# Performance work log

Hardware: AMD Instinct MI355X
Metric: run time of the kernel (lower is better)

Reference implementation:

```python
import jax, jax.numpy as jnp
import numpy as np

EPS = jnp.float16(1e-8)

def setup_inputs() -> dict:
    key = jax.random.key(0)
    k1, k2, k3, k4 = jax.random.split(key, 4)
    B, S, D_IN, D_OUT = 4, 2048, 4096, 4096
    x = jax.random.normal(k1, (B, S, D_IN), dtype=jnp.float16)
    weight = jax.random.randint(k2, (D_OUT, D_IN), -127, 127, dtype=jnp.int32).astype(jnp.int8)
    weight_scales = (jax.random.uniform(k3, (D_OUT,), dtype=jnp.float32) * 0.02 + 0.001).astype(jnp.float16)
    bias = (jax.random.normal(k4, (1, D_OUT), dtype=jnp.float32) * 0.01).astype(jnp.float16)
    return {"x": x, "weight": weight, "weight_scales": weight_scales, "bias": bias}

def fake_quant_per_token(x):
    # per-token absmax fake quant to int8 range, stays fp16
    scales = jnp.max(jnp.abs(x), axis=-1, keepdims=True) / jnp.float16(127.0)
    scales = jnp.maximum(scales, EPS)
    return jnp.round(x / scales) * scales

def reference(x, weight, weight_scales, bias):
    # dequantize int8 weight with per-output-channel scales -> fp16 [out, in]
    w_fp16 = weight.astype(jnp.float16) * weight_scales[:, None]
    xq = fake_quant_per_token(x)
    # y = xq @ w^T + bias  : [B, S, out]
    y = jnp.einsum('bsi,oi->bso', xq, w_fp16) + bias
    return y
```

## Files before the change

### kernel.cpp

```cpp
#include <hip/hip_runtime.h>
#include <hip/hip_fp16.h>
#include <stdint.h>

#define M_TOK 8192
#define KD 4096
#define ND 4096

using i32x4 = __attribute__((ext_vector_type(4))) int;
using f32x4 = __attribute__((ext_vector_type(4))) float;

typedef const __attribute__((address_space(1))) void* gp_t;
typedef __attribute__((address_space(3))) void* lp_t;

__global__ __launch_bounds__(256) void prep_kernel(
    const float* __restrict__ x,
    int8_t* __restrict__ q,
    float* __restrict__ scales,
    const int* __restrict__ w32,
    int8_t* __restrict__ w8)
{
    const int t = threadIdx.x;
    if (blockIdx.x >= 8192) {
        const int b = blockIdx.x - 8192;
        const int4* w4 = (const int4*)w32;
        int* q32 = (int*)w8;
        #pragma unroll
        for (int u = 0; u < 4; ++u) {
            int g = b * 1024 + u * 256 + t;
            int4 a = w4[g];
            q32[g] = (a.x & 255) | ((a.y & 255) << 8) | ((a.z & 255) << 16) | (a.w << 24);
        }
        return;
    }

    const int row  = blockIdx.x;
    const int lane = t & 63;
    const int wave = t >> 6;

    const float4* xr = (const float4*)(x + (size_t)row * KD);
    float4 p[4];
    #pragma unroll
    for (int i = 0; i < 4; ++i) p[i] = xr[i * 256 + t];

    float am = 0.0f;
    #pragma unroll
    for (int i = 0; i < 4; ++i) {
        am = fmaxf(am, fmaxf(fmaxf(fabsf(p[i].x), fabsf(p[i].y)),
                             fmaxf(fabsf(p[i].z), fabsf(p[i].w))));
    }
    #pragma unroll
    for (int off = 32; off >= 1; off >>= 1)
        am = fmaxf(am, __shfl_xor(am, off));

    __shared__ float smax[4];
    if (lane == 0) smax[wave] = am;
    __syncthreads();
    am = fmaxf(fmaxf(smax[0], smax[1]), fmaxf(smax[2], smax[3]));

    float s = __half2float(__float2half(am * (1.0f / 127.0f)));
    s = fmaxf(s, 1e-30f);
    const float inv = 1.0f / s;

    int* qr = (int*)(q + (size_t)row * KD);
    #pragma unroll
    for (int i = 0; i < 4; ++i) {
        float vv[4] = {p[i].x, p[i].y, p[i].z, p[i].w};
        int w32v = 0;
        #pragma unroll
        for (int e = 0; e < 4; ++e) {
            float tq = __half2float(__float2half(vv[e] * inv));
            int qi = (int)rintf(tq);
            qi = max(-127, min(127, qi));
            w32v |= (qi & 255) << (8 * e);
        }
        qr[i * 256 + t] = w32v;
    }
    if (t == 0) scales[row] = s;
}


__device__ __forceinline__ void read_Af(const char* lA, int wr, int lane, i32x4 (&a)[4][2]) {
    const int l15 = lane & 15;
    const int cg  = (lane >> 4) << 4;
    #pragma unroll
    for (int mf = 0; mf < 4; ++mf) {
        const int row = wr * 64 + mf * 16 + l15;
        const int sw  = (row & 7) << 4;
        #pragma unroll
        for (int ks = 0; ks < 2; ++ks)
            a[mf][ks] = *(const i32x4*)(lA + row * 128 + ((ks * 64 + cg) ^ sw));
    }
}

__device__ __forceinline__ void read_Bf(const char* lB, int wc, int lane, i32x4 (&b)[4][2]) {
    const int l15 = lane & 15;
    const int cg  = (lane >> 4) << 4;
    #pragma unroll
    for (int nf = 0; nf < 4; ++nf) {
        const int row = wc * 64 + nf * 16 + l15;
        const int sw  = (row & 7) << 4;
        #pragma unroll
        for (int ks = 0; ks < 2; ++ks)
            b[nf][ks] = *(const i32x4*)(lB + row * 128 + ((ks * 64 + cg) ^ sw));
    }
}

__device__ __forceinline__ void mfma_32(i32x4 (&acc)[4][4],
                                        const i32x4 (&a)[4][2],
                                        const i32x4 (&b)[4][2]) {
    __builtin_amdgcn_s_setprio(1);
    #pragma unroll
    for (int ks = 0; ks < 2; ++ks)
        #pragma unroll
        for (int mf = 0; mf < 4; ++mf)
            #pragma unroll
            for (int nf = 0; nf < 4; ++nf)
                acc[mf][nf] = __builtin_amdgcn_mfma_i32_16x16x64_i8(a[mf][ks], b[nf][ks],
                                                                    acc[mf][nf], 0, 0, 0);
    __builtin_amdgcn_s_setprio(0);
}

#define BAR()   __builtin_amdgcn_s_barrier()
#define LGKM0() asm volatile("s_waitcnt lgkmcnt(0)" ::: "memory")
#define VM8()   asm volatile("s_waitcnt vmcnt(8)")

__global__ __launch_bounds__(256, 2) void gemm_q8_128_kernel(
    const int8_t* __restrict__ q,
    const int8_t* __restrict__ w8,
    const float* __restrict__ qs,
    const float* __restrict__ wscale,
    const float* __restrict__ bias,
    float* __restrict__ y)
{
    __shared__ char lds[2][2][16384];

    const int tid  = threadIdx.x;
    const int lane = tid & 63;
    const int wave = tid >> 6;
    const int wr   = wave >> 1;
    const int wc   = wave & 1;
    const int tn   = blockIdx.x;
    const int tm   = blockIdx.y;

    const int8_t* gA = q  + (size_t)(tm * 128) * KD;
    const int8_t* gB = w8 + (size_t)(tn * 128) * KD;

    char* lA0 = &lds[0][0][0]; char* lB0 = &lds[0][1][0];
    char* lA1 = &lds[1][0][0]; char* lB1 = &lds[1][1][0];

    int goff[4];
    #pragma unroll
    for (int ch = 0; ch < 4; ++ch) {
        const int d = ch * 4096 + tid * 16;
        const int r = d >> 7;
        const int cs = (d & 127) ^ ((r & 7) << 4);
        goff[ch] = r * KD + cs;
    }
    const int ldso = tid * 16;

    #define STAGE(gbase, kbyte, ldst)                                                    \
        do {                                                                             \
            const int8_t* _s = (gbase) + (kbyte);                                        \
            __builtin_amdgcn_global_load_lds((gp_t)(_s + goff[0]), (lp_t)((ldst) + ldso),            16, 0, 0); \
            __builtin_amdgcn_global_load_lds((gp_t)(_s + goff[1]), (lp_t)((ldst) + 4096 + ldso),     16, 0, 0); \
            __builtin_amdgcn_global_load_lds((gp_t)(_s + goff[2]), (lp_t)((ldst) + 8192 + ldso),     16, 0, 0); \
            __builtin_amdgcn_global_load_lds((gp_t)(_s + goff[3]), (lp_t)((ldst) + 12288 + ldso),    16, 0, 0); \
        } while (0)

    i32x4 acc[4][4] = {};
    i32x4 a[4][2], b[4][2];

    STAGE(gA, 0,   lA0);
    STAGE(gB, 0,   lB0);
    STAGE(gA, 128, lA1);
    STAGE(gB, 128, lB1);
    VM8();
    BAR();

    for (int it = 0; it < 16; ++it) {
        const int kt  = 2 * it;
        const int kb2 = ((kt + 2) & 31) * 128;
        const int kb3 = ((kt + 3) & 31) * 128;

        read_Af(lA0, wr, lane, a);
        read_Bf(lB0, wc, lane, b);
        LGKM0();
        BAR();
        STAGE(gA, kb2, lA0);
        STAGE(gB, kb2, lB0);
        mfma_32(acc, a, b);
        VM8();
        BAR();

        read_Af(lA1, wr, lane, a);
        read_Bf(lB1, wc, lane, b);
        LGKM0();
        BAR();
        STAGE(gA, kb3, lA1);
        STAGE(gB, kb3, lB1);
        mfma_32(acc, a, b);
        VM8();
        BAR();
    }
    asm volatile("s_waitcnt vmcnt(0)");
    BAR();

    {
        char* myl = &lds[0][0][0] + wave * 16384;
        const int g   = lane >> 4;
        const int l15 = lane & 15;
        #pragma unroll
        for (int mf = 0; mf < 4; ++mf) {
            const int rmb = tm * 128 + wr * 64 + mf * 16 + g * 4;
            float qsv[4];
            #pragma unroll
            for (int r = 0; r < 4; ++r) qsv[r] = qs[rmb + r];
            #pragma unroll
            for (int nf = 0; nf < 4; ++nf) {
                const int n  = tn * 128 + wc * 64 + nf * 16 + l15;
                const float wn = wscale[n];
                const float bn = bias[n];
                const int cl = nf * 16 + l15;
                #pragma unroll
                for (int r = 0; r < 4; ++r) {
                    const int rl = mf * 16 + g * 4 + r;
                    const float val = (float)acc[mf][nf][r] * (qsv[r] * wn) + bn;
                    *(float*)(myl + rl * 256 + ((cl * 4) ^ ((rl & 7) << 4))) = val;
                }
            }
        }
        __builtin_amdgcn_s_barrier();
        const int gcol = tn * 128 + wc * 64 + l15 * 4;
        #pragma unroll
        for (int k = 0; k < 16; ++k) {
            const int rl = g + k * 4;
            const f32x4 v = *(const f32x4*)(myl + rl * 256 + ((l15 * 16) ^ ((rl & 7) << 4)));
            const int grow = tm * 128 + wr * 64 + rl;
            __builtin_nontemporal_store(v, (f32x4*)(y + (size_t)grow * ND + gcol));
        }
    }
    #undef STAGE
}

__global__ __launch_bounds__(256, 2) void gemm_q8_fallback(
    const int8_t* __restrict__ q,
    const int* __restrict__ w32,
    const float* __restrict__ qs,
    const float* __restrict__ wscale,
    const float* __restrict__ bias,
    float* __restrict__ y)
{
    __shared__ int8_t lA[128 * 64];
    __shared__ int8_t lB[128 * 64];

    const int tid  = threadIdx.x;
    const int lane = tid & 63;
    const int wave = tid >> 6;
    const int wr   = wave >> 1;
    const int wc   = wave & 1;
    const int tn   = blockIdx.x;
    const int tm   = blockIdx.y;

    const int ci0  = wave * 2;
    const int off0 = ci0 * 1024 + lane * 16;
    const int r0   = off0 >> 6;
    const int c0   = off0 & 63;
    const int off1 = off0 + 1024;
    const int r1   = off1 >> 6;
    const int c1   = off1 & 63;

    const int8_t* gA0 = q + (size_t)(tm * 128 + r0) * KD + c0;
    const int8_t* gA1 = q + (size_t)(tm * 128 + r1) * KD + c1;

    const int brow  = tid >> 1;
    const int bhalf = tid & 1;
    const int* gW = w32 + (size_t)(tn * 128 + brow) * KD + bhalf * 32;

    i32x4 acc[4][4] = {};
    const int kc = (lane >> 4) * 16;
    const int rA = wr * 64 + (lane & 15);
    const int rB = wc * 64 + (lane & 15);

    for (int k0 = 0; k0 < KD; k0 += 64) {
        __builtin_amdgcn_global_load_lds((gp_t)(gA0 + k0), (lp_t)(lA + ci0 * 1024),        16, 0, 0);
        __builtin_amdgcn_global_load_lds((gp_t)(gA1 + k0), (lp_t)(lA + ci0 * 1024 + 1024), 16, 0, 0);
        int bw[8];
        #pragma unroll
        for (int u = 0; u < 8; ++u) {
            i32x4 a4 = *(const i32x4*)(gW + k0 + u * 4);
            bw[u] = (a4[0] & 255) | ((a4[1] & 255) << 8) | ((a4[2] & 255) << 16) | (a4[3] << 24);
        }
        *(i32x4*)(lB + brow * 64 + bhalf * 32)      = i32x4{bw[0], bw[1], bw[2], bw[3]};
        *(i32x4*)(lB + brow * 64 + bhalf * 32 + 16) = i32x4{bw[4], bw[5], bw[6], bw[7]};
        __syncthreads();

        i32x4 a[4], b[4];
        #pragma unroll
        for (int i = 0; i < 4; ++i) a[i] = *(const i32x4*)(lA + (rA + i * 16) * 64 + kc);
        #pragma unroll
        for (int j = 0; j < 4; ++j) b[j] = *(const i32x4*)(lB + (rB + j * 16) * 64 + kc);
        #pragma unroll
        for (int i = 0; i < 4; ++i)
            #pragma unroll
            for (int j = 0; j < 4; ++j)
                acc[i][j] = __builtin_amdgcn_mfma_i32_16x16x64_i8(a[i], b[j], acc[i][j], 0, 0, 0);
        __syncthreads();
    }

    const int cbase = tn * 128 + wc * 64 + (lane & 15);
    const int rbase = tm * 128 + wr * 64 + ((lane >> 4) << 2);
    #pragma unroll
    for (int j = 0; j < 4; ++j) {
        const int n  = cbase + j * 16;
        const float wn = wscale[n];
        const float bn = bias[n];
        #pragma unroll
        for (int i = 0; i < 4; ++i)
            #pragma unroll
            for (int r = 0; r < 4; ++r) {
                const int m = rbase + i * 16 + r;
                y[(size_t)m * ND + n] = (float)acc[i][j][r] * (qs[m] * wn) + bn;
            }
    }
}

extern "C" void kernel_launch(void* const* d_in, const int* in_sizes, int n_in,
                              void* d_out, int out_size, void* d_ws, size_t ws_size,
                              hipStream_t stream) {
    const float* x      = (const float*)d_in[0];
    const int*   w32    = (const int*)d_in[1];
    const float* wscale = (const float*)d_in[2];
    const float* bias   = (const float*)d_in[3];
    float*       y      = (float*)d_out;

    const size_t q_bytes  = (size_t)M_TOK * KD;
    const size_t s_bytes  = (size_t)M_TOK * sizeof(float);
    const size_t w8_bytes = (size_t)ND * KD;

    int8_t* qbuf   = (int8_t*)d_ws;
    float*  scales = (float*)((char*)d_ws + q_bytes);
    int8_t* w8     = (int8_t*)((char*)d_ws + q_bytes + s_bytes);

    if (ws_size >= q_bytes + s_bytes + w8_bytes) {
        prep_kernel<<<8192 + 4096, 256, 0, stream>>>(x, qbuf, scales, w32, w8);
        dim3 grid(ND / 128, M_TOK / 128);
        gemm_q8_128_kernel<<<grid, 256, 0, stream>>>(qbuf, w8, scales, wscale, bias, y);
    } else {
        prep_kernel<<<8192, 256, 0, stream>>>(x, qbuf, scales, w32, w8);
        dim3 grid(ND / 128, M_TOK / 128);
        gemm_q8_fallback<<<grid, 256, 0, stream>>>(qbuf, w32, scales, wscale, bias, y);
    }
}
```

Before: 174.0 us.

## Enlarge GEMM tile to 256x128 with K=64 stages and swizzled block order

```diff
diff --git a/kernel.cpp b/kernel.cpp
--- a/kernel.cpp
+++ b/kernel.cpp
@@ -79,52 +79,23 @@
 }
 
 
-__device__ __forceinline__ void read_Af(const char* lA, int wr, int lane, i32x4 (&a)[4][2]) {
-    const int l15 = lane & 15;
-    const int cg  = (lane >> 4) << 4;
-    #pragma unroll
-    for (int mf = 0; mf < 4; ++mf) {
-        const int row = wr * 64 + mf * 16 + l15;
-        const int sw  = (row & 7) << 4;
-        #pragma unroll
-        for (int ks = 0; ks < 2; ++ks)
-            a[mf][ks] = *(const i32x4*)(lA + row * 128 + ((ks * 64 + cg) ^ sw));
-    }
-}
-
-__device__ __forceinline__ void read_Bf(const char* lB, int wc, int lane, i32x4 (&b)[4][2]) {
-    const int l15 = lane & 15;
-    const int cg  = (lane >> 4) << 4;
-    #pragma unroll
-    for (int nf = 0; nf < 4; ++nf) {
-        const int row = wc * 64 + nf * 16 + l15;
-        const int sw  = (row & 7) << 4;
-        #pragma unroll
-        for (int ks = 0; ks < 2; ++ks)
-            b[nf][ks] = *(const i32x4*)(lB + row * 128 + ((ks * 64 + cg) ^ sw));
-    }
-}
-
-__device__ __forceinline__ void mfma_32(i32x4 (&acc)[4][4],
-                                        const i32x4 (&a)[4][2],
-                                        const i32x4 (&b)[4][2]) {
+__device__ __forceinline__ void mfma_32(i32x4 (&acc)[8][4],
+                                        const i32x4 (&a)[8],
+                                        const i32x4 (&b)[4]) {
     __builtin_amdgcn_s_setprio(1);
     #pragma unroll
-    for (int ks = 0; ks < 2; ++ks)
-        #pragma unroll
-        for (int mf = 0; mf < 4; ++mf)
-            #pragma unroll
-            for (int nf = 0; nf < 4; ++nf)
-                acc[mf][nf] = __builtin_amdgcn_mfma_i32_16x16x64_i8(a[mf][ks], b[nf][ks],
-                                                                    acc[mf][nf], 0, 0, 0);
+    for (int mf = 0; mf < 8; ++mf)
+        #pragma unroll
+        for (int nf = 0; nf < 4; ++nf)
+            acc[mf][nf] = __builtin_amdgcn_mfma_i32_16x16x64_i8(a[mf], b[nf], acc[mf][nf], 0, 0, 0);
     __builtin_amdgcn_s_setprio(0);
 }
 
 #define BAR()   __builtin_amdgcn_s_barrier()
 #define LGKM0() asm volatile("s_waitcnt lgkmcnt(0)" ::: "memory")
-#define VM8()   asm volatile("s_waitcnt vmcnt(8)")
-
-__global__ __launch_bounds__(256, 2) void gemm_q8_128_kernel(
+#define VM6()   asm volatile("s_waitcnt vmcnt(6)")
+
+__global__ __launch_bounds__(256, 2) void gemm_q8_hrb_kernel(
     const int8_t* __restrict__ q,
     const int8_t* __restrict__ w8,
     const float* __restrict__ qs,
@@ -132,114 +103,155 @@
     const float* __restrict__ bias,
     float* __restrict__ y)
 {
-    __shared__ char lds[2][2][16384];
+    __shared__ char lds[2][24576];
 
     const int tid  = threadIdx.x;
     const int lane = tid & 63;
     const int wave = tid >> 6;
     const int wr   = wave >> 1;
     const int wc   = wave & 1;
-    const int tn   = blockIdx.x;
-    const int tm   = blockIdx.y;
-
-    const int8_t* gA = q  + (size_t)(tm * 128) * KD;
+
+    const int bid = blockIdx.x;
+    const int sid = (bid & 7) * 128 + (bid >> 3);
+    const int tn  = sid & 31;
+    const int tm  = sid >> 5;
+
+    const int8_t* gA = q  + (size_t)(tm * 256) * KD;
     const int8_t* gB = w8 + (size_t)(tn * 128) * KD;
 
-    char* lA0 = &lds[0][0][0]; char* lB0 = &lds[0][1][0];
-    char* lA1 = &lds[1][0][0]; char* lB1 = &lds[1][1][0];
+    const int l15 = lane & 15;
+    const int cg  = (lane >> 4) << 4;
+    const int swz = ((l15 >> 1) & 7) << 4;
+    const int c0  = (cg + 64 * (l15 & 1)) ^ swz;
+    unsigned aoff[8], boff[4];
+    #pragma unroll
+    for (int mf = 0; mf < 8; ++mf)
+        aoff[mf] = (unsigned)((wr * 64 + mf * 8 + (l15 >> 1)) * 128 + c0);
+    #pragma unroll
+    for (int nf = 0; nf < 4; ++nf)
+        boff[nf] = (unsigned)((wc * 32 + nf * 8 + (l15 >> 1)) * 128 + c0);
 
     int goff[4];
     #pragma unroll
     for (int ch = 0; ch < 4; ++ch) {
-        const int d = ch * 4096 + tid * 16;
-        const int r = d >> 7;
-        const int cs = (d & 127) ^ ((r & 7) << 4);
-        goff[ch] = r * KD + cs;
+        const int d  = ch * 4096 + tid * 16;
+        const int i  = d >> 7;
+        const int sp = (d >> 4) & 7;
+        const int s  = sp ^ (i & 7);
+        const int r  = 2 * i + (s >> 2);
+        const int k  = (s & 3) * 16;
+        goff[ch] = r * KD + k;
     }
     const int ldso = tid * 16;
 
-    #define STAGE(gbase, kbyte, ldst)                                                    \
+    #define STAGE(kbyte, buf)                                                                         \
+        do {                                                                                          \
+            char* _lA = &lds[buf][0];                                                                 \
+            char* _lB = &lds[buf][16384];                                                             \
+            __builtin_amdgcn_global_load_lds((gp_t)(gA + (kbyte) + goff[0]), (lp_t)(_lA + ldso),          16, 0, 0); \
+            __builtin_amdgcn_global_load_lds((gp_t)(gA + (kbyte) + goff[1]), (lp_t)(_lA + 4096 + ldso),   16, 0, 0); \
+            __builtin_amdgcn_global_load_lds((gp_t)(gA + (kbyte) + goff[2]), (lp_t)(_lA + 8192 + ldso),   16, 0, 0); \
+            __builtin_amdgcn_global_load_lds((gp_t)(gA + (kbyte) + goff[3]), (lp_t)(_lA + 12288 + ldso),  16, 0, 0); \
+            __builtin_amdgcn_global_load_lds((gp_t)(gB + (kbyte) + goff[0]), (lp_t)(_lB + ldso),          16, 0, 0); \
+            __builtin_amdgcn_global_load_lds((gp_t)(gB + (kbyte) + goff[1]), (lp_t)(_lB + 4096 + ldso),   16, 0, 0); \
+        } while (0)
+
+    #define READS(buf)                                                                   \
         do {                                                                             \
-            const int8_t* _s = (gbase) + (kbyte);                                        \
-            __builtin_amdgcn_global_load_lds((gp_t)(_s + goff[0]), (lp_t)((ldst) + ldso),            16, 0, 0); \
-            __builtin_amdgcn_global_load_lds((gp_t)(_s + goff[1]), (lp_t)((ldst) + 4096 + ldso),     16, 0, 0); \
-            __builtin_amdgcn_global_load_lds((gp_t)(_s + goff[2]), (lp_t)((ldst) + 8192 + ldso),     16, 0, 0); \
-            __builtin_amdgcn_global_load_lds((gp_t)(_s + goff[3]), (lp_t)((ldst) + 12288 + ldso),    16, 0, 0); \
+            const char* _lA = &lds[buf][0];                                              \
+            const char* _lB = &lds[buf][16384];                                          \
+            _Pragma("unroll")                                                            \
+            for (int mf = 0; mf < 8; ++mf) a[mf] = *(const i32x4*)(_lA + aoff[mf]);      \
+            _Pragma("unroll")                                                            \
+            for (int nf = 0; nf < 4; ++nf) b[nf] = *(const i32x4*)(_lB + boff[nf]);      \
         } while (0)
 
-    i32x4 acc[4][4] = {};
-    i32x4 a[4][2], b[4][2];
-
-    STAGE(gA, 0,   lA0);
-    STAGE(gB, 0,   lB0);
-    STAGE(gA, 128, lA1);
-    STAGE(gB, 128, lB1);
-    VM8();
-    BAR();
-
-    for (int it = 0; it < 16; ++it) {
-        const int kt  = 2 * it;
-        const int kb2 = ((kt + 2) & 31) * 128;
-        const int kb3 = ((kt + 3) & 31) * 128;
-
-        read_Af(lA0, wr, lane, a);
-        read_Bf(lB0, wc, lane, b);
+    i32x4 acc[8][4] = {};
+    i32x4 a[8], b[4];
+
+    STAGE(0,  0);
+    STAGE(64, 1);
+    VM6();
+    BAR();
+
+    for (int it = 0; it < 31; ++it) {
+        const int kb2 = (2 * it + 2) * 64;
+        const int kb3 = (2 * it + 3) * 64;
+
+        READS(0);
         LGKM0();
         BAR();
-        STAGE(gA, kb2, lA0);
-        STAGE(gB, kb2, lB0);
+        STAGE(kb2, 0);
         mfma_32(acc, a, b);
-        VM8();
+        VM6();
         BAR();
 
-        read_Af(lA1, wr, lane, a);
-        read_Bf(lB1, wc, lane, b);
+        READS(1);
         LGKM0();
         BAR();
-        STAGE(gA, kb3, lA1);
-        STAGE(gB, kb3, lB1);
+        STAGE(kb3, 1);
         mfma_32(acc, a, b);
-        VM8();
+        VM6();
         BAR();
     }
+
+    READS(0);
+    LGKM0();
+    BAR();
+    mfma_32(acc, a, b);
     asm volatile("s_waitcnt vmcnt(0)");
     BAR();
 
+    READS(1);
+    LGKM0();
+    BAR();
+    mfma_32(acc, a, b);
+    BAR();
+
     {
-        char* myl = &lds[0][0][0] + wave * 16384;
-        const int g   = lane >> 4;
-        const int l15 = lane & 15;
-        #pragma unroll
-        for (int mf = 0; mf < 4; ++mf) {
-            const int rmb = tm * 128 + wr * 64 + mf * 16 + g * 4;
-            float qsv[4];
-            #pragma unroll
-            for (int r = 0; r < 4; ++r) qsv[r] = qs[rmb + r];
-            #pragma unroll
-            for (int nf = 0; nf < 4; ++nf) {
-                const int n  = tn * 128 + wc * 64 + nf * 16 + l15;
-                const float wn = wscale[n];
-                const float bn = bias[n];
-                const int cl = nf * 16 + l15;
+        char* eld = &lds[0][0];
+        const int g = lane >> 4;
+        #pragma unroll
+        for (int p = 0; p < 4; ++p) {
+            if (wr == (p >> 1)) {
                 #pragma unroll
-                for (int r = 0; r < 4; ++r) {
-                    const int rl = mf * 16 + g * 4 + r;
-                    const float val = (float)acc[mf][nf][r] * (qsv[r] * wn) + bn;
-                    *(float*)(myl + rl * 256 + ((cl * 4) ^ ((rl & 7) << 4))) = val;
+                for (int mq = 0; mq < 4; ++mq) {
+                    const int mf  = (p & 1) * 4 + mq;
+                    const int rmb = tm * 256 + wr * 128 + mf * 16 + g * 4;
+                    float qsv[4];
+                    #pragma unroll
+                    for (int r = 0; r < 4; ++r) qsv[r] = qs[rmb + r];
+                    #pragma unroll
+                    for (int nf = 0; nf < 4; ++nf) {
+                        const int n  = tn * 128 + wc * 64 + nf * 16 + l15;
+                        const float wn = wscale[n];
+                        const float bn = bias[n];
+                        const int cl = wc * 64 + nf * 16 + l15;
+                        #pragma unroll
+                        for (int r = 0; r < 4; ++r) {
+                            const int rl = mq * 16 + g * 4 + r;
+                            const float val = (float)acc[mf][nf][r] * (qsv[r] * wn) + bn;
+                            *(float*)(eld + rl * 512 + ((cl * 4) ^ ((rl & 31) << 4))) = val;
+                        }
+                    }
                 }
             }
+            __builtin_amdgcn_s_barrier();
+            const int c32 = tid & 31;
+            const int r8  = tid >> 5;
+            const int gcol = tn * 128 + c32 * 4;
+            #pragma unroll
+            for (int k = 0; k < 8; ++k) {
+                const int rl = r8 + k * 8;
+                const f32x4 v = *(const f32x4*)(eld + rl * 512 + ((c32 * 16) ^ ((rl & 31) << 4)));
+                const int grow = tm * 256 + p * 64 + rl;
+                __builtin_nontemporal_store(v, (f32x4*)(y + (size_t)grow * ND + gcol));
+            }
+            __builtin_amdgcn_s_barrier();
         }
-        __builtin_amdgcn_s_barrier();
-        const int gcol = tn * 128 + wc * 64 + l15 * 4;
-        #pragma unroll
-        for (int k = 0; k < 16; ++k) {
-            const int rl = g + k * 4;
-            const f32x4 v = *(const f32x4*)(myl + rl * 256 + ((l15 * 16) ^ ((rl & 7) << 4)));
-            const int grow = tm * 128 + wr * 64 + rl;
-            __builtin_nontemporal_store(v, (f32x4*)(y + (size_t)grow * ND + gcol));
-        }
     }
     #undef STAGE
+    #undef READS
 }
 
 __global__ __launch_bounds__(256, 2) void gemm_q8_fallback(
@@ -343,8 +355,7 @@
 
     if (ws_size >= q_bytes + s_bytes + w8_bytes) {
         prep_kernel<<<8192 + 4096, 256, 0, stream>>>(x, qbuf, scales, w32, w8);
-        dim3 grid(ND / 128, M_TOK / 128);
-        gemm_q8_128_kernel<<<grid, 256, 0, stream>>>(qbuf, w8, scales, wscale, bias, y);
+        gemm_q8_hrb_kernel<<<1024, 256, 0, stream>>>(qbuf, w8, scales, wscale, bias, y);
     } else {
         prep_kernel<<<8192, 256, 0, stream>>>(x, qbuf, scales, w32, w8);
         dim3 grid(ND / 128, M_TOK / 128);
```

New measurement: 185.5 us. 1.07x slower.

## Restructure int8 GEMM mainloop into triple-buffered K=64 pipeline with register prefetch

Applied to the files above, without the earlier changes.

```diff
diff --git a/kernel.cpp b/kernel.cpp
--- a/kernel.cpp
+++ b/kernel.cpp
@@ -79,52 +79,9 @@
 }
 
 
-__device__ __forceinline__ void read_Af(const char* lA, int wr, int lane, i32x4 (&a)[4][2]) {
-    const int l15 = lane & 15;
-    const int cg  = (lane >> 4) << 4;
-    #pragma unroll
-    for (int mf = 0; mf < 4; ++mf) {
-        const int row = wr * 64 + mf * 16 + l15;
-        const int sw  = (row & 7) << 4;
-        #pragma unroll
-        for (int ks = 0; ks < 2; ++ks)
-            a[mf][ks] = *(const i32x4*)(lA + row * 128 + ((ks * 64 + cg) ^ sw));
-    }
-}
-
-__device__ __forceinline__ void read_Bf(const char* lB, int wc, int lane, i32x4 (&b)[4][2]) {
-    const int l15 = lane & 15;
-    const int cg  = (lane >> 4) << 4;
-    #pragma unroll
-    for (int nf = 0; nf < 4; ++nf) {
-        const int row = wc * 64 + nf * 16 + l15;
-        const int sw  = (row & 7) << 4;
-        #pragma unroll
-        for (int ks = 0; ks < 2; ++ks)
-            b[nf][ks] = *(const i32x4*)(lB + row * 128 + ((ks * 64 + cg) ^ sw));
-    }
-}
-
-__device__ __forceinline__ void mfma_32(i32x4 (&acc)[4][4],
-                                        const i32x4 (&a)[4][2],
-                                        const i32x4 (&b)[4][2]) {
-    __builtin_amdgcn_s_setprio(1);
-    #pragma unroll
-    for (int ks = 0; ks < 2; ++ks)
-        #pragma unroll
-        for (int mf = 0; mf < 4; ++mf)
-            #pragma unroll
-            for (int nf = 0; nf < 4; ++nf)
-                acc[mf][nf] = __builtin_amdgcn_mfma_i32_16x16x64_i8(a[mf][ks], b[nf][ks],
-                                                                    acc[mf][nf], 0, 0, 0);
-    __builtin_amdgcn_s_setprio(0);
-}
-
-#define BAR()   __builtin_amdgcn_s_barrier()
-#define LGKM0() asm volatile("s_waitcnt lgkmcnt(0)" ::: "memory")
-#define VM8()   asm volatile("s_waitcnt vmcnt(8)")
-
-__global__ __launch_bounds__(256, 2) void gemm_q8_128_kernel(
+#define BAR() __builtin_amdgcn_s_barrier()
+
+__global__ __launch_bounds__(256, 2) void gemm_q8_pipe_kernel(
     const int8_t* __restrict__ q,
     const int8_t* __restrict__ w8,
     const float* __restrict__ qs,
@@ -132,7 +89,7 @@
     const float* __restrict__ bias,
     float* __restrict__ y)
 {
-    __shared__ char lds[2][2][16384];
+    __shared__ char lds[3][16384];
 
     const int tid  = threadIdx.x;
     const int lane = tid & 63;
@@ -145,101 +102,155 @@
     const int8_t* gA = q  + (size_t)(tm * 128) * KD;
     const int8_t* gB = w8 + (size_t)(tn * 128) * KD;
 
-    char* lA0 = &lds[0][0][0]; char* lB0 = &lds[0][1][0];
-    char* lA1 = &lds[1][0][0]; char* lB1 = &lds[1][1][0];
-
-    int goff[4];
-    #pragma unroll
-    for (int ch = 0; ch < 4; ++ch) {
+    const int l15 = lane & 15;
+    const int cg  = (lane >> 4) << 4;
+    const int csw = cg ^ ((l15 & 3) << 4);
+    unsigned aoff[4], boff[4];
+    #pragma unroll
+    for (int f = 0; f < 4; ++f) {
+        aoff[f] = (unsigned)((wr * 64 + f * 16 + l15) * 64 + csw);
+        boff[f] = (unsigned)((wc * 64 + f * 16 + l15) * 64 + csw);
+    }
+
+    int goff[2];
+    #pragma unroll
+    for (int ch = 0; ch < 2; ++ch) {
         const int d = ch * 4096 + tid * 16;
-        const int r = d >> 7;
-        const int cs = (d & 127) ^ ((r & 7) << 4);
-        goff[ch] = r * KD + cs;
+        const int r = d >> 6;
+        const int sp = (d >> 4) & 3;
+        const int s  = sp ^ (r & 3);
+        goff[ch] = r * KD + (s << 4);
     }
     const int ldso = tid * 16;
 
-    #define STAGE(gbase, kbyte, ldst)                                                    \
+    #define STAGE(kbyte, bufi)                                                                        \
+        do {                                                                                          \
+            char* _lA = &lds[bufi][0];                                                                \
+            char* _lB = &lds[bufi][8192];                                                             \
+            __builtin_amdgcn_global_load_lds((gp_t)(gA + (kbyte) + goff[0]), (lp_t)(_lA + ldso),         16, 0, 0); \
+            __builtin_amdgcn_global_load_lds((gp_t)(gA + (kbyte) + goff[1]), (lp_t)(_lA + 4096 + ldso),  16, 0, 0); \
+            __builtin_amdgcn_global_load_lds((gp_t)(gB + (kbyte) + goff[0]), (lp_t)(_lB + ldso),         16, 0, 0); \
+            __builtin_amdgcn_global_load_lds((gp_t)(gB + (kbyte) + goff[1]), (lp_t)(_lB + 4096 + ldso),  16, 0, 0); \
+        } while (0)
+
+    #define RD(FA_, FB_, bufi)                                                           \
         do {                                                                             \
-            const int8_t* _s = (gbase) + (kbyte);                                        \
-            __builtin_amdgcn_global_load_lds((gp_t)(_s + goff[0]), (lp_t)((ldst) + ldso),            16, 0, 0); \
-            __builtin_amdgcn_global_load_lds((gp_t)(_s + goff[1]), (lp_t)((ldst) + 4096 + ldso),     16, 0, 0); \
-            __builtin_amdgcn_global_load_lds((gp_t)(_s + goff[2]), (lp_t)((ldst) + 8192 + ldso),     16, 0, 0); \
-            __builtin_amdgcn_global_load_lds((gp_t)(_s + goff[3]), (lp_t)((ldst) + 12288 + ldso),    16, 0, 0); \
+            const char* _lA = &lds[bufi][0];                                             \
+            const char* _lB = &lds[bufi][8192];                                          \
+            _Pragma("unroll")                                                            \
+            for (int f = 0; f < 4; ++f) FA_[f] = *(const i32x4*)(_lA + aoff[f]);         \
+            _Pragma("unroll")                                                            \
+            for (int f = 0; f < 4; ++f) FB_[f] = *(const i32x4*)(_lB + boff[f]);         \
         } while (0)
 
+    #define MFMA16(FA_, FB_)                                                             \
+        do {                                                                             \
+            __builtin_amdgcn_s_setprio(1);                                               \
+            _Pragma("unroll")                                                            \
+            for (int mf = 0; mf < 4; ++mf)                                               \
+                _Pragma("unroll")                                                        \
+                for (int nf = 0; nf < 4; ++nf)                                           \
+                    acc[mf][nf] = __builtin_amdgcn_mfma_i32_16x16x64_i8(FA_[mf], FB_[nf], acc[mf][nf], 0, 0, 0); \
+            __builtin_amdgcn_s_setprio(0);                                               \
+        } while (0)
+
+    #define PHASE(nb, sb, FNa, FNb, FCa, FCb, kst)                                       \
+        do {                                                                             \
+            RD(FNa, FNb, nb);                                                            \
+            asm volatile("s_waitcnt lgkmcnt(8)" ::: "memory");                           \
+            __builtin_amdgcn_sched_barrier(0);                                           \
+            BAR();                                                                       \
+            STAGE((kst) * 64, sb);                                                       \
+            MFMA16(FCa, FCb);                                                            \
+            asm volatile("s_waitcnt vmcnt(4)");                                          \
+            BAR();                                                                       \
+        } while (0)
+
     i32x4 acc[4][4] = {};
-    i32x4 a[4][2], b[4][2];
-
-    STAGE(gA, 0,   lA0);
-    STAGE(gB, 0,   lB0);
-    STAGE(gA, 128, lA1);
-    STAGE(gB, 128, lB1);
-    VM8();
+    i32x4 f0a[4], f0b[4], f1a[4], f1b[4];
+
+    STAGE(0,   0);
+    STAGE(64,  1);
+    STAGE(128, 2);
+    asm volatile("s_waitcnt vmcnt(4)");
     BAR();
-
-    for (int it = 0; it < 16; ++it) {
-        const int kt  = 2 * it;
-        const int kb2 = ((kt + 2) & 31) * 128;
-        const int kb3 = ((kt + 3) & 31) * 128;
-
-        read_Af(lA0, wr, lane, a);
-        read_Bf(lB0, wc, lane, b);
-        LGKM0();
-        BAR();
-        STAGE(gA, kb2, lA0);
-        STAGE(gB, kb2, lB0);
-        mfma_32(acc, a, b);
-        VM8();
-        BAR();
-
-        read_Af(lA1, wr, lane, a);
-        read_Bf(lB1, wc, lane, b);
-        LGKM0();
-        BAR();
-        STAGE(gA, kb3, lA1);
-        STAGE(gB, kb3, lB1);
-        mfma_32(acc, a, b);
-        VM8();
-        BAR();
-    }
-    asm volatile("s_waitcnt vmcnt(0)");
-    BAR();
-
+    RD(f0a, f0b, 0);
+
+    for (int it = 0; it < 10; ++it) {
+        const int kt = 6 * it;
+        PHASE(1, 0, f1a, f1b, f0a, f0b, kt + 3);
+        PHASE(2, 1, f0a, f0b, f1a, f1b, kt + 4);
+        PHASE(0, 2, f1a, f1b, f0a, f0b, kt + 5);
+        PHASE(1, 0, f0a, f0b, f1a, f1b, kt + 6);
+        PHASE(2, 1, f1a, f1b, f0a, f0b, kt + 7);
+        PHASE(0, 2, f0a, f0b, f1a, f1b, kt + 8);
+    }
+
+    PHASE(1, 0, f1a, f1b, f0a, f0b, 63);
     {
-        char* myl = &lds[0][0][0] + wave * 16384;
-        const int g   = lane >> 4;
-        const int l15 = lane & 15;
-        #pragma unroll
-        for (int mf = 0; mf < 4; ++mf) {
-            const int rmb = tm * 128 + wr * 64 + mf * 16 + g * 4;
-            float qsv[4];
+        RD(f0a, f0b, 2);
+        asm volatile("s_waitcnt lgkmcnt(8)" ::: "memory");
+        __builtin_amdgcn_sched_barrier(0);
+        BAR();
+        MFMA16(f1a, f1b);
+        asm volatile("s_waitcnt vmcnt(0)");
+        BAR();
+
+        RD(f1a, f1b, 0);
+        asm volatile("s_waitcnt lgkmcnt(8)" ::: "memory");
+        __builtin_amdgcn_sched_barrier(0);
+        BAR();
+        MFMA16(f0a, f0b);
+        BAR();
+
+        asm volatile("s_waitcnt lgkmcnt(0)" ::: "memory");
+        __builtin_amdgcn_sched_barrier(0);
+        MFMA16(f1a, f1b);
+        BAR();
+    }
+
+    {
+        char* eld = &lds[0][0] + wave * 8192;
+        const int g = lane >> 4;
+        #pragma unroll
+        for (int h = 0; h < 2; ++h) {
             #pragma unroll
-            for (int r = 0; r < 4; ++r) qsv[r] = qs[rmb + r];
-            #pragma unroll
-            for (int nf = 0; nf < 4; ++nf) {
-                const int n  = tn * 128 + wc * 64 + nf * 16 + l15;
-                const float wn = wscale[n];
-                const float bn = bias[n];
-                const int cl = nf * 16 + l15;
+            for (int mq = 0; mq < 2; ++mq) {
+                const int mf  = h * 2 + mq;
+                const int rmb = tm * 128 + wr * 64 + mf * 16 + g * 4;
+                float qsv[4];
                 #pragma unroll
-                for (int r = 0; r < 4; ++r) {
-                    const int rl = mf * 16 + g * 4 + r;
-                    const float val = (float)acc[mf][nf][r] * (qsv[r] * wn) + bn;
-                    *(float*)(myl + rl * 256 + ((cl * 4) ^ ((rl & 7) << 4))) = val;
+                for (int r = 0; r < 4; ++r) qsv[r] = qs[rmb + r];
+                #pragma unroll
+                for (int nf = 0; nf < 4; ++nf) {
+                    const int n  = tn * 128 + wc * 64 + nf * 16 + l15;
+                    const float wn = wscale[n];
+                    const float bn = bias[n];
+                    const int cl = nf * 16 + l15;
+                    #pragma unroll
+                    for (int r = 0; r < 4; ++r) {
+                        const int rl = mq * 16 + g * 4 + r;
+                        const float val = (float)acc[mf][nf][r] * (qsv[r] * wn) + bn;
+                        *(float*)(eld + rl * 256 + ((cl * 4) ^ ((rl & 7) << 4))) = val;
+                    }
                 }
             }
+            __builtin_amdgcn_s_barrier();
+            const int gcol = tn * 128 + wc * 64 + l15 * 4;
+            #pragma unroll
+            for (int k = 0; k < 8; ++k) {
+                const int rl = g + k * 4;
+                const f32x4 v = *(const f32x4*)(eld + rl * 256 + ((l15 * 16) ^ ((rl & 7) << 4)));
+                const int grow = tm * 128 + wr * 64 + h * 32 + rl;
+                __builtin_nontemporal_store(v, (f32x4*)(y + (size_t)grow * ND + gcol));
+            }
+            __builtin_amdgcn_s_barrier();
         }
-        __builtin_amdgcn_s_barrier();
-        const int gcol = tn * 128 + wc * 64 + l15 * 4;
-        #pragma unroll
-        for (int k = 0; k < 16; ++k) {
-            const int rl = g + k * 4;
-            const f32x4 v = *(const f32x4*)(myl + rl * 256 + ((l15 * 16) ^ ((rl & 7) << 4)));
-            const int grow = tm * 128 + wr * 64 + rl;
-            __builtin_nontemporal_store(v, (f32x4*)(y + (size_t)grow * ND + gcol));
-        }
     }
     #undef STAGE
+    #undef RD
+    #undef MFMA16
+    #undef PHASE
 }
 
 __global__ __launch_bounds__(256, 2) void gemm_q8_fallback(
@@ -344,7 +355,7 @@
     if (ws_size >= q_bytes + s_bytes + w8_bytes) {
         prep_kernel<<<8192 + 4096, 256, 0, stream>>>(x, qbuf, scales, w32, w8);
         dim3 grid(ND / 128, M_TOK / 128);
-        gemm_q8_128_kernel<<<grid, 256, 0, stream>>>(qbuf, w8, scales, wscale, bias, y);
+        gemm_q8_pipe_kernel<<<grid, 256, 0, stream>>>(qbuf, w8, scales, wscale, bias, y);
     } else {
         prep_kernel<<<8192, 256, 0, stream>>>(x, qbuf, scales, w32, w8);
         dim3 grid(ND / 128, M_TOK / 128);
```

Result: slower. 200.7 us (+15.3%).
